# Kernel optimization log

Measured on AMD Instinct MI355X. Metric: run time of the kernel, lower is better.

## Reference

```python
import jax, jax.numpy as jnp
import numpy as np
from jax import lax

V, E, HD, B, S, T = 50000, 256, 512, 32, 256, 24
H = HD // 2  # per-direction hidden size


def setup_inputs() -> dict:
    key = jax.random.key(0)
    ks = jax.random.split(key, 15)
    def n(k, shape, scale=0.1):
        return jax.random.normal(k, shape, jnp.float32) * scale
    return dict(
        sentence=jax.random.randint(ks[0], (B, S), 0, V),
        embed=n(ks[1], (V, E)),
        Wih_f=n(ks[2], (4 * H, E)), Whh_f=n(ks[3], (4 * H, H)),
        bih_f=n(ks[4], (4 * H,)), bhh_f=n(ks[5], (4 * H,)),
        Wih_b=n(ks[6], (4 * H, E)), Whh_b=n(ks[7], (4 * H, H)),
        bih_b=n(ks[8], (4 * H,)), bhh_b=n(ks[9], (4 * H,)),
        Wout=n(ks[10], (T, HD)), bout=n(ks[11], (T,)),
        transitions=n(ks[12], (T, T), 1.0),
        start_t=n(ks[13], (T,), 1.0),
        stop_t=n(ks[14], (T,), 1.0),
    )


def _lstm_dir(xs, Wih, Whh, bih, bhh, reverse):
    # xs: [S, B, E] -> hs: [S, B, H]; PyTorch gate order i,f,g,o
    bsz, hh = xs.shape[1], Whh.shape[1]
    x_proj = jnp.einsum('sbe,ge->sbg', xs, Wih) + bih + bhh  # [S,B,4H]
    def step(carry, xp):
        h, c = carry
        gates = xp + h @ Whh.T
        i, f, g, o = jnp.split(gates, 4, axis=-1)
        c = jax.nn.sigmoid(f) * c + jax.nn.sigmoid(i) * jnp.tanh(g)
        h = jax.nn.sigmoid(o) * jnp.tanh(c)
        return (h, c), h
    init = (jnp.zeros((bsz, hh), xs.dtype), jnp.zeros((bsz, hh), xs.dtype))
    _, hs = lax.scan(step, init, x_proj, reverse=reverse)
    return hs


def _features(sentence, embed, Wih_f, Whh_f, bih_f, bhh_f,
              Wih_b, Whh_b, bih_b, bhh_b, Wout, bout):
    emb = embed[sentence]                      # [B,S,E]
    xs = jnp.swapaxes(emb, 0, 1)               # [S,B,E]
    hf = _lstm_dir(xs, Wih_f, Whh_f, bih_f, bhh_f, reverse=False)
    hb = _lstm_dir(xs, Wih_b, Whh_b, bih_b, bhh_b, reverse=True)
    hs = jnp.concatenate([hf, hb], axis=-1)    # [S,B,HD]
    return jnp.einsum('sbh,th->sbt', hs, Wout) + bout  # [S,B,T]


def reference(sentence, embed, Wih_f, Whh_f, bih_f, bhh_f,
              Wih_b, Whh_b, bih_b, bhh_b, Wout, bout,
              transitions, start_t, stop_t):
    feats = _features(sentence, embed, Wih_f, Whh_f, bih_f, bhh_f,
                      Wih_b, Whh_b, bih_b, bhh_b, Wout, bout)  # [S,B,T]
    # Viterbi decode (faithful to _viterbi_decode)
    v0 = feats[0] + start_t[None, :]           # [B,T]
    def step(v, feat):
        scores = v[:, :, None] + transitions[None]  # [B, prev T, next T]
        idx = jnp.argmax(scores, axis=1)       # [B,T] best previous tag
        v = jnp.max(scores, axis=1) + feat
        return v, idx
    v, idxs = lax.scan(step, v0, feats[1:])    # idxs: [S-1,B,T]
    last = jnp.argmax(v + stop_t[None, :], axis=1)  # [B]
    def back(tag, idx):
        tag = jnp.take_along_axis(idx, tag[:, None], axis=1)[:, 0]
        return tag, tag
    _, prev_tags = lax.scan(back, last, idxs, reverse=True)  # [S-1,B]
    tags = jnp.concatenate([prev_tags, last[None]], axis=0)  # [S,B]
    return jnp.swapaxes(tags, 0, 1)            # [B,S]
```

## Files before the change

### kernel.cpp

```cpp
#include <hip/hip_runtime.h>
#include <hip/hip_bf16.h>


#define S_LEN 256
#define BATCH 32
#define NTAG  24

__global__ __launch_bounds__(256) void k_prep(
    const float* __restrict__ WhhF, const float* __restrict__ WhhB,
    float* __restrict__ Wt) {
  int idx = blockIdx.x * 256 + threadIdx.x;
  int dir = idx >> 18;
  int r = idx & 262143;
  int k = r >> 10;
  int jg = r & 1023;
  int j = jg >> 2, g = jg & 3;
  const float* W = dir ? WhhB : WhhF;
  Wt[idx] = W[(size_t)(g * 256 + j) * 256 + k];
}

__global__ __launch_bounds__(256) void k_inproj(
    const int* __restrict__ sent, const float* __restrict__ embed,
    const float* __restrict__ WihF, const float* __restrict__ bihF, const float* __restrict__ bhhF,
    const float* __restrict__ WihB, const float* __restrict__ bihB, const float* __restrict__ bhhB,
    float* __restrict__ xq) {
  int tm = blockIdx.x;
  int tn = blockIdx.y;
  int dir = blockIdx.z;
  const float* Wih = dir ? WihB : WihF;
  const float* bih = dir ? bihB : bihF;
  const float* bhh = dir ? bhhB : bhhF;
  __shared__ float As[64 * 36];
  __shared__ float Bs[64 * 36];
  __shared__ int toks[64];
  int tid = threadIdx.x;
  if (tid < 64) {
    int r = tm * 64 + tid;
    int s = r >> 5, b = r & 31;
    toks[tid] = sent[b * S_LEN + s];
  }
  __syncthreads();
  int mt = tid & 15, nt = tid >> 4;
  float acc[4][4] = {};
  for (int k0 = 0; k0 < 256; k0 += 32) {
    for (int it = 0; it < 2; ++it) {
      int u = it * 256 + tid;
      int row = u >> 3, lf = u & 7;
      float4 av = *(const float4*)&embed[(size_t)toks[row] * 256 + k0 + lf * 4];
      *(float4*)&As[row * 36 + lf * 4] = av;
      int grow = tn * 64 + row;
      float4 wv = *(const float4*)&Wih[(size_t)grow * 256 + k0 + lf * 4];
      *(float4*)&Bs[row * 36 + lf * 4] = wv;
    }
    __syncthreads();
#pragma unroll
    for (int kc = 0; kc < 8; ++kc) {
      float4 a[4], w[4];
#pragma unroll
      for (int i = 0; i < 4; ++i) a[i] = *(const float4*)&As[(mt + 16 * i) * 36 + kc * 4];
#pragma unroll
      for (int j = 0; j < 4; ++j) w[j] = *(const float4*)&Bs[(nt + 16 * j) * 36 + kc * 4];
#pragma unroll
      for (int i = 0; i < 4; ++i)
#pragma unroll
        for (int j = 0; j < 4; ++j)
          acc[i][j] += a[i].x * w[j].x + a[i].y * w[j].y + a[i].z * w[j].z + a[i].w * w[j].w;
    }
    __syncthreads();
  }
#pragma unroll
  for (int i = 0; i < 4; ++i) {
    int r = tm * 64 + mt + 16 * i;
    int s = r >> 5, b = r & 31;
#pragma unroll
    for (int j = 0; j < 4; ++j) {
      int gg = tn * 64 + nt + 16 * j;
      float v = acc[i][j] + bih[gg] + bhh[gg];
      xq[(((size_t)(dir * 32 + b)) * 256 + s) * 1024 + (gg & 255) * 4 + (gg >> 8)] = v;
    }
  }
}

__global__ __launch_bounds__(256, 1) void k_lstm(
    const float* __restrict__ Wt,
    const float* __restrict__ xq,
    float* __restrict__ hX,
    float* __restrict__ hsF,
    unsigned int* __restrict__ flags) {
  int B = blockIdx.x;
  int q = (B >> 3) & 3;
  int gid = (B & 7) | ((B >> 5) << 3);
  int dir = gid >> 5;
  int b = gid & 31;
  int tid = threadIdx.x;
  int w = tid >> 6;
  int l = tid & 63;
  int kbase = w * 64;
  int unit = q * 64 + l;

  __shared__ float red[4][64 * 8];

  float4 wreg[64];
  {
    const float* wp = Wt + ((size_t)dir * 256 + kbase) * 1024 + unit * 4;
#pragma unroll
    for (int kk = 0; kk < 64; ++kk)
      wreg[kk] = *(const float4*)(wp + (size_t)kk * 1024);
  }

  float c_st = 0.f;
  const unsigned int* fl = flags + gid * 32 + (tid & 3);

#pragma unroll 1
  for (int t = 0; t < 256; ++t) {
    int s = dir ? (255 - t) : t;
    int par = t & 1;

    float4 xv = {0.f, 0.f, 0.f, 0.f};
    if (w == 0)
      xv = *(const float4*)&xq[(((size_t)(dir * 32 + b)) * 256 + s) * 1024 + unit * 4];

    {
      unsigned spins = 0;
      while (true) {
        unsigned v = __hip_atomic_load(fl, __ATOMIC_RELAXED, __HIP_MEMORY_SCOPE_AGENT);
        if (__all(v >= (unsigned)t)) break;
        __builtin_amdgcn_s_sleep(1);
        if (++spins > (1u << 21)) break;
      }
    }

    float hval;
    {
      const float* hp = hX + (((size_t)par * 2 + dir) * 32 + b) * 256;
      hval = __hip_atomic_load(&hp[kbase + l], __ATOMIC_RELAXED, __HIP_MEMORY_SCOPE_AGENT);
    }

    float4 acc = {0.f, 0.f, 0.f, 0.f};
#pragma unroll
    for (int kk = 0; kk < 64; ++kk) {
      float hk = __shfl(hval, kk);
      acc.x += wreg[kk].x * hk;
      acc.y += wreg[kk].y * hk;
      acc.z += wreg[kk].z * hk;
      acc.w += wreg[kk].w * hk;
    }
    *(float4*)&red[w][l * 8] = acc;
    __syncthreads();

    if (w == 0) {
      float4 r0 = *(const float4*)&red[0][l * 8];
      float4 r1 = *(const float4*)&red[1][l * 8];
      float4 r2 = *(const float4*)&red[2][l * 8];
      float4 r3 = *(const float4*)&red[3][l * 8];
      float xi = r0.x + r1.x + r2.x + r3.x + xv.x;
      float xf = r0.y + r1.y + r2.y + r3.y + xv.y;
      float xg = r0.z + r1.z + r2.z + r3.z + xv.z;
      float xo = r0.w + r1.w + r2.w + r3.w + xv.w;
      float si = 1.f / (1.f + expf(-xi));
      float sf = 1.f / (1.f + expf(-xf));
      float so = 1.f / (1.f + expf(-xo));
      float tg = tanhf(xg);
      c_st = sf * c_st + si * tg;
      float h = so * tanhf(c_st);
      float* hn = hX + (((size_t)(par ^ 1) * 2 + dir) * 32 + b) * 256;
      __hip_atomic_store(&hn[unit], h, __ATOMIC_RELAXED, __HIP_MEMORY_SCOPE_AGENT);
      hsF[(((size_t)(dir * 32 + b)) * 256 + s) * 256 + unit] = h;
      asm volatile("s_waitcnt vmcnt(0)" ::: "memory");
      if (l == 0)
        __hip_atomic_store(&flags[gid * 32 + q], (unsigned)(t + 1),
                           __ATOMIC_RELAXED, __HIP_MEMORY_SCOPE_AGENT);
    }
  }
}

__global__ __launch_bounds__(256) void k_feats(
    const float* __restrict__ hsF, const float* __restrict__ Wout,
    const float* __restrict__ bout, float* __restrict__ feats) {
  int s = blockIdx.x;
  int tid = threadIdx.x;
  __shared__ float Hl[32 * 260];
  __shared__ float Wl[24 * 260];
  float acc[3] = {};
  for (int dir = 0; dir < 2; ++dir) {
    __syncthreads();
    for (int u = tid; u < 8192; u += 256) {
      int b = u >> 8, j = u & 255;
      Hl[b * 260 + j] = hsF[(((size_t)(dir * 32 + b)) * 256 + s) * 256 + j];
    }
    for (int u = tid; u < 24 * 256; u += 256) {
      int t = u >> 8, j = u & 255;
      Wl[t * 260 + j] = Wout[t * 512 + dir * 256 + j];
    }
    __syncthreads();
    int b = tid & 31, th = tid >> 5;
    for (int jc = 0; jc < 64; ++jc) {
      float4 hv = *(const float4*)&Hl[b * 260 + jc * 4];
#pragma unroll
      for (int rep = 0; rep < 3; ++rep) {
        int t = rep * 8 + th;
        float4 wv = *(const float4*)&Wl[t * 260 + jc * 4];
        acc[rep] += hv.x * wv.x + hv.y * wv.y + hv.z * wv.z + hv.w * wv.w;
      }
    }
  }
  int b = tid & 31, th = tid >> 5;
#pragma unroll
  for (int rep = 0; rep < 3; ++rep) {
    int t = rep * 8 + th;
    feats[((size_t)s * 32 + b) * 24 + t] = acc[rep] + bout[t];
  }
}

__global__ __launch_bounds__(64) void k_viterbi(
    const float* __restrict__ feats, const float* __restrict__ trans,
    const float* __restrict__ start_t, const float* __restrict__ stop_t,
    int* __restrict__ out) {
  int b = blockIdx.x;
  int j = threadIdx.x;
  bool act = j < NTAG;
  int j2 = act ? j : 0;
  __shared__ unsigned char idxL[255 * 24];
  __shared__ float sv[32];
  float tr[24];
#pragma unroll
  for (int i = 0; i < 24; ++i) tr[i] = trans[i * 24 + j2];
  float vj = feats[(size_t)b * 24 + j2] + start_t[j2];
  if (!act) vj = -1e30f;
#pragma unroll 1
  for (int s = 1; s < 256; ++s) {
    float m = -1e30f;
    int arg = 0;
#pragma unroll
    for (int i = 0; i < 24; ++i) {
      float vi = __shfl(vj, i);
      float sc = vi + tr[i];
      if (sc > m) { m = sc; arg = i; }
    }
    float fj = feats[((size_t)s * 32 + b) * 24 + j2];
    if (act) {
      idxL[(s - 1) * 24 + j] = (unsigned char)arg;
      vj = m + fj;
    }
  }
  if (act) sv[j] = vj + stop_t[j];
  __syncthreads();
  if (j == 0) {
    float m = sv[0];
    int tag = 0;
    for (int i = 1; i < 24; ++i)
      if (sv[i] > m) { m = sv[i]; tag = i; }
    out[b * 256 + 255] = tag;
    for (int s = 254; s >= 0; --s) {
      tag = idxL[s * 24 + tag];
      out[b * 256 + s] = tag;
    }
  }
}

extern "C" void kernel_launch(void* const* d_in, const int* in_sizes, int n_in,
                              void* d_out, int out_size, void* d_ws, size_t ws_size,
                              hipStream_t stream) {
  const int*   sent   = (const int*)  d_in[0];
  const float* embed  = (const float*)d_in[1];
  const float* WihF   = (const float*)d_in[2];
  const float* WhhF   = (const float*)d_in[3];
  const float* bihF   = (const float*)d_in[4];
  const float* bhhF   = (const float*)d_in[5];
  const float* WihB   = (const float*)d_in[6];
  const float* WhhB   = (const float*)d_in[7];
  const float* bihB   = (const float*)d_in[8];
  const float* bhhB   = (const float*)d_in[9];
  const float* Wout   = (const float*)d_in[10];
  const float* bout   = (const float*)d_in[11];
  const float* trans  = (const float*)d_in[12];
  const float* startt = (const float*)d_in[13];
  const float* stopt  = (const float*)d_in[14];
  int* out = (int*)d_out;

  char* ws = (char*)d_ws;
  size_t off = 0;
  float* xq = (float*)(ws + off);           off += (size_t)2 * 32 * 256 * 1024 * 4;
  size_t off_sync = off;
  float* hX = (float*)(ws + off);           off += (size_t)2 * 2 * 32 * 256 * 4;
  unsigned int* flags = (unsigned int*)(ws + off); off += (size_t)64 * 32 * 4;
  size_t sync_len = off - off_sync;
  float* hsF = (float*)(ws + off);          off += (size_t)2 * 32 * 256 * 256 * 4;
  float* feats = (float*)(ws + off);        off += (size_t)256 * 32 * 24 * 4;
  float* Wt = (float*)(ws + off);           off += (size_t)2 * 256 * 1024 * 4;

  hipMemsetAsync(ws + off_sync, 0, sync_len, stream);

  k_prep<<<2048, 256, 0, stream>>>(WhhF, WhhB, Wt);
  k_inproj<<<dim3(128, 16, 2), 256, 0, stream>>>(sent, embed, WihF, bihF, bhhF,
                                                 WihB, bihB, bhhB, xq);
  k_lstm<<<256, 256, 0, stream>>>(Wt, xq, hX, hsF, flags);
  k_feats<<<256, 256, 0, stream>>>(hsF, Wout, bout, feats);
  k_viterbi<<<32, 64, 0, stream>>>(feats, trans, startt, stopt, out);
}
```

Before: 1.280 ms.

## Pack hidden value with step tag into 64-bit atomics for inter-block sync

Replaces the separate per-block flag array and its polling with 64-bit words that carry the hidden-state float together with the timestep number. Each consumer lane spins directly on its own h element until the tag matches, so the producer's vmcnt(0) wait and the second flag store, plus the extra load round trip after the flag check, are removed. The sleep in the spin loop is also dropped and the spin cap lowered. The cost is doubled storage for the h exchange and more polling traffic on the shared words.

Result: faster. 1.128 ms (-11.9%).

```diff
diff --git a/kernel.cpp b/kernel.cpp
--- a/kernel.cpp
+++ b/kernel.cpp
@@ -84,9 +84,8 @@
 __global__ __launch_bounds__(256, 1) void k_lstm(
     const float* __restrict__ Wt,
     const float* __restrict__ xq,
-    float* __restrict__ hX,
-    float* __restrict__ hsF,
-    unsigned int* __restrict__ flags) {
+    unsigned long long* __restrict__ hX2,
+    float* __restrict__ hsF) {
   int B = blockIdx.x;
   int q = (B >> 3) & 3;
   int gid = (B & 7) | ((B >> 5) << 3);
@@ -109,31 +108,27 @@
   }
 
   float c_st = 0.f;
-  const unsigned int* fl = flags + gid * 32 + (tid & 3);
 
 #pragma unroll 1
   for (int t = 0; t < 256; ++t) {
     int s = dir ? (255 - t) : t;
-    int par = t & 1;
 
     float4 xv = {0.f, 0.f, 0.f, 0.f};
     if (w == 0)
       xv = *(const float4*)&xq[(((size_t)(dir * 32 + b)) * 256 + s) * 1024 + unit * 4];
 
+    float hval;
     {
+      const unsigned long long* hp =
+          hX2 + ((((size_t)(t & 1) * 2 + dir) * 32 + b) * 256 + kbase + l);
+      unsigned long long a;
       unsigned spins = 0;
       while (true) {
-        unsigned v = __hip_atomic_load(fl, __ATOMIC_RELAXED, __HIP_MEMORY_SCOPE_AGENT);
-        if (__all(v >= (unsigned)t)) break;
-        __builtin_amdgcn_s_sleep(1);
-        if (++spins > (1u << 21)) break;
+        a = __hip_atomic_load(hp, __ATOMIC_RELAXED, __HIP_MEMORY_SCOPE_AGENT);
+        if (__all((unsigned)(a >> 32) == (unsigned)t)) break;
+        if (++spins > (1u << 18)) break;
       }
-    }
-
-    float hval;
-    {
-      const float* hp = hX + (((size_t)par * 2 + dir) * 32 + b) * 256;
-      hval = __hip_atomic_load(&hp[kbase + l], __ATOMIC_RELAXED, __HIP_MEMORY_SCOPE_AGENT);
+      hval = __uint_as_float((unsigned)a);
     }
 
     float4 acc = {0.f, 0.f, 0.f, 0.f};
@@ -163,13 +158,13 @@
       float tg = tanhf(xg);
       c_st = sf * c_st + si * tg;
       float h = so * tanhf(c_st);
-      float* hn = hX + (((size_t)(par ^ 1) * 2 + dir) * 32 + b) * 256;
-      __hip_atomic_store(&hn[unit], h, __ATOMIC_RELAXED, __HIP_MEMORY_SCOPE_AGENT);
+      unsigned long long atom =
+          ((unsigned long long)(unsigned)(t + 1) << 32) |
+          (unsigned long long)__float_as_uint(h);
+      unsigned long long* hn =
+          hX2 + ((((size_t)((t + 1) & 1) * 2 + dir) * 32 + b) * 256 + unit);
+      __hip_atomic_store(hn, atom, __ATOMIC_RELAXED, __HIP_MEMORY_SCOPE_AGENT);
       hsF[(((size_t)(dir * 32 + b)) * 256 + s) * 256 + unit] = h;
-      asm volatile("s_waitcnt vmcnt(0)" ::: "memory");
-      if (l == 0)
-        __hip_atomic_store(&flags[gid * 32 + q], (unsigned)(t + 1),
-                           __ATOMIC_RELAXED, __HIP_MEMORY_SCOPE_AGENT);
     }
   }
 }
@@ -282,8 +277,8 @@
   size_t off = 0;
   float* xq = (float*)(ws + off);           off += (size_t)2 * 32 * 256 * 1024 * 4;
   size_t off_sync = off;
-  float* hX = (float*)(ws + off);           off += (size_t)2 * 2 * 32 * 256 * 4;
-  unsigned int* flags = (unsigned int*)(ws + off); off += (size_t)64 * 32 * 4;
+  unsigned long long* hX2 = (unsigned long long*)(ws + off);
+                                            off += (size_t)2 * 2 * 32 * 256 * 8;
   size_t sync_len = off - off_sync;
   float* hsF = (float*)(ws + off);          off += (size_t)2 * 32 * 256 * 256 * 4;
   float* feats = (float*)(ws + off);        off += (size_t)256 * 32 * 24 * 4;
@@ -294,7 +289,7 @@
   k_prep<<<2048, 256, 0, stream>>>(WhhF, WhhB, Wt);
   k_inproj<<<dim3(128, 16, 2), 256, 0, stream>>>(sent, embed, WihF, bihF, bhhF,
                                                  WihB, bihB, bhhB, xq);
-  k_lstm<<<256, 256, 0, stream>>>(Wt, xq, hX, hsF, flags);
+  k_lstm<<<256, 256, 0, stream>>>(Wt, xq, hX2, hsF);
   k_feats<<<256, 256, 0, stream>>>(hsF, Wout, bout, feats);
   k_viterbi<<<32, 64, 0, stream>>>(feats, trans, startt, stopt, out);
 }
```
